# Kernel tuning notes

Hardware: AMD Instinct MI355X
Metric: run time of the kernel (lower is better)

The kernel has to match this reference:

```python
import jax, jax.numpy as jnp
import numpy as np

N, E, G = 50000, 640000, 256
NODE_IN, EDGE_IN, EXT_IN = 32, 16, 8
H, L = 128, 3
BN_EPS = 1e-5


def _linear_init(key, fan_in, fan_out):
    kw, kb = jax.random.split(key)
    s = 1.0 / np.sqrt(fan_in)
    w = jax.random.uniform(kw, (fan_in, fan_out), minval=-s, maxval=s, dtype=jnp.float32)
    b = jax.random.uniform(kb, (fan_out,), minval=-s, maxval=s, dtype=jnp.float32)
    return w, b


def setup_inputs() -> dict:
    key = jax.random.key(0)
    ks = jax.random.split(key, 16)
    x = jax.random.normal(ks[0], (N, NODE_IN), dtype=jnp.float32)
    edge_index = jax.random.randint(ks[1], (2, E), 0, N)
    edge_attr = jax.random.normal(ks[2], (E, EDGE_IN), dtype=jnp.float32)
    batch = jnp.sort(jax.random.randint(ks[3], (N,), 0, G))
    externals = jax.random.normal(ks[4], (G, EXT_IN), dtype=jnp.float32)

    node_w, node_b = _linear_init(ks[5], NODE_IN, H)
    ee_w1, ee_b1 = _linear_init(ks[6], EDGE_IN, H)
    ee_w2, ee_b2 = _linear_init(ks[7], H, H)
    # stacked per-layer GINEConv MLP params: [L, H, H] / [L, H]
    cks = jax.random.split(ks[8], 2 * L)
    cw1, cb1, cw2, cb2 = [], [], [], []
    for l in range(L):
        w1, b1 = _linear_init(cks[2 * l], H, H)
        w2, b2 = _linear_init(cks[2 * l + 1], H, H)
        cw1.append(w1); cb1.append(b1); cw2.append(w2); cb2.append(b2)
    conv_w1 = jnp.stack(cw1); conv_b1 = jnp.stack(cb1)
    conv_w2 = jnp.stack(cw2); conv_b2 = jnp.stack(cb2)
    bn_gamma = jnp.ones((L, H), dtype=jnp.float32)
    bn_beta = jnp.zeros((L, H), dtype=jnp.float32)
    ext_w1, ext_b1 = _linear_init(ks[9], EXT_IN, H)
    ext_w2, ext_b2 = _linear_init(ks[10], H, H)
    reg_w1, reg_b1 = _linear_init(ks[11], 2 * H, H)
    reg_w2, reg_b2 = _linear_init(ks[12], H, 1)

    return dict(x=x, edge_attr=edge_attr, externals=externals,
                node_w=node_w, node_b=node_b,
                ee_w1=ee_w1, ee_b1=ee_b1, ee_w2=ee_w2, ee_b2=ee_b2,
                conv_w1=conv_w1, conv_b1=conv_b1, conv_w2=conv_w2, conv_b2=conv_b2,
                bn_gamma=bn_gamma, bn_beta=bn_beta,
                ext_w1=ext_w1, ext_b1=ext_b1, ext_w2=ext_w2, ext_b2=ext_b2,
                reg_w1=reg_w1, reg_b1=reg_b1, reg_w2=reg_w2, reg_b2=reg_b2,
                edge_index=edge_index, batch=batch, num_graphs=G)


def reference(x, edge_attr, externals,
              node_w, node_b, ee_w1, ee_b1, ee_w2, ee_b2,
              conv_w1, conv_b1, conv_w2, conv_b2, bn_gamma, bn_beta,
              ext_w1, ext_b1, ext_w2, ext_b2,
              reg_w1, reg_b1, reg_w2, reg_b2,
              edge_index, batch, num_graphs):
    n = x.shape[0]
    src, dst = edge_index[0], edge_index[1]
    h = x @ node_w + node_b                                      # [N,H]
    e = jax.nn.relu(edge_attr @ ee_w1 + ee_b1) @ ee_w2 + ee_b2   # [E,H]
    for l in range(conv_w1.shape[0]):
        # GINEConv (eps=0): aggr = sum_j relu(x_j + e_ij); out = MLP(x_i + aggr)
        msg = jax.nn.relu(h[src] + e)                            # gather + add + relu [E,H]
        aggr = jax.ops.segment_sum(msg, dst, num_segments=n)     # scatter-add [N,H]
        z = h + aggr
        z = jax.nn.relu(z @ conv_w1[l] + conv_b1[l]) @ conv_w2[l] + conv_b2[l]
        # BatchNorm1d (batch statistics)
        mean = z.mean(axis=0)
        var = z.var(axis=0)
        z = (z - mean) * jax.lax.rsqrt(var + BN_EPS) * bn_gamma[l] + bn_beta[l]
        h = jax.nn.relu(z)                                       # dropout = identity (eval)
    # global mean pool over graphs
    gsum = jax.ops.segment_sum(h, batch, num_segments=num_graphs)
    cnt = jax.ops.segment_sum(jnp.ones((n, 1), h.dtype), batch, num_segments=num_graphs)
    graph_emb = gsum / jnp.maximum(cnt, 1.0)
    ext = jax.nn.relu(externals @ ext_w1 + ext_b1) @ ext_w2 + ext_b2
    comb = jnp.concatenate([graph_emb, ext], axis=-1)            # [G,2H]
    out = jax.nn.relu(comb @ reg_w1 + reg_b1) @ reg_w2 + reg_b2  # [G,1]
    return out.squeeze(-1)
```

## Files before the change

### kernel.cpp

```cpp
#include <hip/hip_runtime.h>

typedef __bf16 bf16_t;
typedef __bf16 bf16x8 __attribute__((ext_vector_type(8)));
typedef __bf16 bf16x4 __attribute__((ext_vector_type(4)));
typedef __bf16 bf16x2 __attribute__((ext_vector_type(2)));
typedef float  f32x4  __attribute__((ext_vector_type(4)));

#define MFMA16(a, b, c) __builtin_amdgcn_mfma_f32_16x16x32_bf16((a), (b), (c), 0, 0, 0)

__global__ __launch_bounds__(256) void prep_all_kernel(
    const float* __restrict__ nw,  const float* __restrict__ ew1,
    const float* __restrict__ ew2, const float* __restrict__ cw1,
    const float* __restrict__ cw2,
    bf16_t* __restrict__ nwt,  bf16_t* __restrict__ ew1t,
    bf16_t* __restrict__ ew2t, bf16_t* __restrict__ cw1t,
    bf16_t* __restrict__ cw2t)
{
    int b = blockIdx.x;
    const float* W; bf16_t* O; int Kact, KP, lb;
    if (b < 16)       { W = nw;  O = nwt;  Kact = 32;  KP = 32;  lb = b; }
    else if (b < 32)  { W = ew1; O = ew1t; Kact = 16;  KP = 32;  lb = b - 16; }
    else if (b < 96)  { W = ew2; O = ew2t; Kact = 128; KP = 128; lb = b - 32; }
    else if (b < 288) { int l = (b - 96) / 64;  W = cw1 + l * 16384; O = cw1t + l * 16384;
                        Kact = 128; KP = 128; lb = (b - 96) % 64; }
    else              { int l = (b - 288) / 64; W = cw2 + l * 16384; O = cw2t + l * 16384;
                        Kact = 128; KP = 128; lb = (b - 288) % 64; }
    int idx = lb * 256 + threadIdx.x;
    if (idx >= 128 * KP) return;
    int j    = idx & 7;
    int lane = (idx >> 3) & 63;
    int ct   = (idx >> 9) & 7;
    int kc   = idx >> 12;
    int n = ct * 16 + (lane & 15);
    int k = kc * 32 + (lane >> 4) * 8 + j;
    O[idx] = (bf16_t)((k < Kact) ? W[k * 128 + n] : 0.0f);
}

__global__ __launch_bounds__(256) void hist_kernel(const int* __restrict__ ei,
                                                   int* __restrict__ deg, int E,
                                                   const float* __restrict__ ea) {
    int t = blockIdx.x * 256 + threadIdx.x;
    if (t < E) {
        atomicAdd(&deg[ei[(long)E + t]], 1);
        float w0 = ea[(long)t * 16];
        float w1 = ea[(long)t * 16 + 8];
        asm volatile("" :: "v"(w0), "v"(w1));
    }
}

__global__ __launch_bounds__(256) void scanA_kernel(const int* __restrict__ deg,
                                                    int* __restrict__ partials,
                                                    int* __restrict__ bsums, int N) {
    __shared__ int s[256];
    int b = blockIdx.x, t = threadIdx.x;
    int base = b * 1024 + t * 4;
    int v0 = (base + 0 < N) ? deg[base + 0] : 0;
    int v1 = (base + 1 < N) ? deg[base + 1] : 0;
    int v2 = (base + 2 < N) ? deg[base + 2] : 0;
    int v3 = (base + 3 < N) ? deg[base + 3] : 0;
    int local = v0 + v1 + v2 + v3;
    s[t] = local;
    __syncthreads();
    for (int off = 1; off < 256; off <<= 1) {
        int v = (t >= off) ? s[t - off] : 0;
        __syncthreads();
        s[t] += v;
        __syncthreads();
    }
    int excl = s[t] - local;
    if (base + 0 < N) partials[base + 0] = excl;
    if (base + 1 < N) partials[base + 1] = excl + v0;
    if (base + 2 < N) partials[base + 2] = excl + v0 + v1;
    if (base + 3 < N) partials[base + 3] = excl + v0 + v1 + v2;
    if (t == 255) bsums[b] = s[255];
}

__global__ __launch_bounds__(256) void scanB_kernel(const int* __restrict__ bsums,
                                                    int* __restrict__ boff,
                                                    int* __restrict__ rowptr,
                                                    int NB, int N) {
    __shared__ int s[256];
    int t = threadIdx.x;
    int local = (t < NB) ? bsums[t] : 0;
    s[t] = local;
    __syncthreads();
    for (int off = 1; off < 256; off <<= 1) {
        int v = (t >= off) ? s[t - off] : 0;
        __syncthreads();
        s[t] += v;
        __syncthreads();
    }
    if (t < NB) boff[t] = s[t] - local;
    if (t == NB - 1) rowptr[N] = s[t];
}

__global__ __launch_bounds__(256) void scanC_kernel(const int* __restrict__ partials,
                                                    const int* __restrict__ boff,
                                                    int* __restrict__ rowptr,
                                                    int* __restrict__ cursor, int N) {
    int i = blockIdx.x * 256 + threadIdx.x;
    if (i >= N) return;
    int v = partials[i] + boff[i >> 10];
    rowptr[i] = v;
    cursor[i] = v;
}

__global__ __launch_bounds__(256) void scatter_kernel(const int* __restrict__ ei,
                                                      int* __restrict__ cursor,
                                                      int* __restrict__ srcp,
                                                      int* __restrict__ eorig, int E) {
    int t = blockIdx.x * 256 + threadIdx.x;
    if (t >= E) return;
    int d = ei[(long)E + t];
    int pos = atomicAdd(&cursor[d], 1);
    srcp[pos] = ei[t];
    eorig[pos] = t;
}

__global__ __launch_bounds__(256) void node_enc_kernel(
    const float* __restrict__ A, int M,
    const bf16_t* __restrict__ Ws, const float* __restrict__ bias,
    bf16_t* __restrict__ outp)
{
    constexpr int S = 136;
    __shared__ bf16_t T[128 * S];

    const int  tid  = threadIdx.x;
    const int  wv   = tid >> 6, lane = tid & 63;
    const long row0 = (long)blockIdx.x * 128;
    const int  l16  = lane & 15, quad = lane >> 4;

    {
        int r  = wv * 32 + (lane >> 1);
        long gr = row0 + r;
        int c0 = (lane & 1) * 16;
#pragma unroll
        for (int q = 0; q < 4; ++q) {
            float4 v = make_float4(0.f, 0.f, 0.f, 0.f);
            if (gr < M) v = *(const float4*)(A + gr * 32 + c0 + q * 4);
            bf16_t* d = &T[r * S + c0 + q * 4];
            d[0] = (bf16_t)v.x; d[1] = (bf16_t)v.y; d[2] = (bf16_t)v.z; d[3] = (bf16_t)v.w;
        }
    }

    f32x4 acc[2][8];
#pragma unroll
    for (int r = 0; r < 2; r++)
#pragma unroll
        for (int c = 0; c < 8; c++) acc[r][c] = (f32x4){0.f, 0.f, 0.f, 0.f};

    {
        bf16x8 af0 = *(const bf16x8*)&T[(wv * 32 + l16) * S + quad * 8];
        bf16x8 af1 = *(const bf16x8*)&T[(wv * 32 + 16 + l16) * S + quad * 8];
#pragma unroll
        for (int c = 0; c < 8; c++) {
            bf16x8 bfr = *(const bf16x8*)&Ws[((c * 64) + lane) * 8];
            acc[0][c] = MFMA16(af0, bfr, acc[0][c]);
            acc[1][c] = MFMA16(af1, bfr, acc[1][c]);
        }
    }

#pragma unroll
    for (int r = 0; r < 2; r++) {
        int mrow = wv * 32 + r * 16 + quad * 4;
#pragma unroll
        for (int c = 0; c < 8; c++) {
            int col = c * 16 + l16;
            float bb = bias[col];
#pragma unroll
            for (int q = 0; q < 4; q++)
                T[(mrow + q) * S + col] = (bf16_t)(acc[r][c][q] + bb);
        }
    }

#pragma unroll
    for (int it = 0; it < 8; ++it) {
        int idx = it * 64 + lane;
        int row = wv * 32 + (idx >> 4);
        int seg = idx & 15;
        long grow = row0 + row;
        if (grow < M)
            *(uint4*)&outp[grow * 128 + seg * 8] = *(const uint4*)&T[row * S + seg * 8];
    }
}

__global__ __launch_bounds__(256) void edge_mlp_kernel(
    const float* __restrict__ A, int M,
    const bf16_t* __restrict__ Ws1, const float* __restrict__ b1,
    const bf16_t* __restrict__ Ws2, const float* __restrict__ b2,
    const int* __restrict__ eorig, bf16_t* __restrict__ outp)
{
    constexpr int S = 136;
    __shared__ bf16_t T[64 * S];

    const int  tid  = threadIdx.x;
    const int  wv   = tid >> 6, lane = tid & 63;
    const long row0 = (long)blockIdx.x * 64;
    const int  l16  = lane & 15, quad = lane >> 4;

    {
        int  r  = wv * 16 + (lane >> 2);
        long gr = row0 + r;
        float4 v = make_float4(0.f, 0.f, 0.f, 0.f);
        if (gr < M) {
            long eo = eorig[gr];
            v = *(const float4*)(A + eo * 16 + (lane & 3) * 4);
        }
        bf16_t* d = &T[r * S + (lane & 3) * 4];
        d[0] = (bf16_t)v.x; d[1] = (bf16_t)v.y; d[2] = (bf16_t)v.z; d[3] = (bf16_t)v.w;
    }

    f32x4 acc[8];
#pragma unroll
    for (int c = 0; c < 8; c++) acc[c] = (f32x4){0.f, 0.f, 0.f, 0.f};

    {
        bf16x8 af;
#pragma unroll
        for (int j = 0; j < 8; ++j) af[j] = (bf16_t)0.f;
        if (quad < 2) af = *(const bf16x8*)&T[(wv * 16 + l16) * S + quad * 8];
#pragma unroll
        for (int c = 0; c < 8; c++) {
            bf16x8 bfr = *(const bf16x8*)&Ws1[((c * 64) + lane) * 8];
            acc[c] = MFMA16(af, bfr, acc[c]);
        }
    }

    const int mbase = wv * 16 + quad * 4;

#pragma unroll
    for (int c = 0; c < 8; c++) {
        int col = c * 16 + l16;
        float bb = b1[col];
#pragma unroll
        for (int q = 0; q < 4; q++)
            T[(mbase + q) * S + col] = (bf16_t)fmaxf(acc[c][q] + bb, 0.f);
    }

#pragma unroll
    for (int c = 0; c < 8; c++) acc[c] = (f32x4){0.f, 0.f, 0.f, 0.f};

#pragma unroll
    for (int kc = 0; kc < 4; ++kc) {
        bf16x8 af = *(const bf16x8*)&T[(wv * 16 + l16) * S + kc * 32 + quad * 8];
#pragma unroll
        for (int c = 0; c < 8; c++) {
            bf16x8 bfr = *(const bf16x8*)&Ws2[(((kc * 8 + c) * 64) + lane) * 8];
            acc[c] = MFMA16(af, bfr, acc[c]);
        }
    }

#pragma unroll
    for (int c = 0; c < 8; c++) {
        int col = c * 16 + l16;
        float bb = b2[col];
#pragma unroll
        for (int q = 0; q < 4; q++)
            T[(mbase + q) * S + col] = (bf16_t)(acc[c][q] + bb);
    }

#pragma unroll
    for (int it = 0; it < 4; ++it) {
        int idx = it * 64 + lane;
        int row = wv * 16 + (idx >> 4);
        int seg = idx & 15;
        long grow = row0 + row;
        if (grow < M)
            *(uint4*)&outp[grow * 128 + seg * 8] = *(const uint4*)&T[row * S + seg * 8];
    }
}

template <int BN>
__global__ __launch_bounds__(512) void aggr_conv_kernel(
    const bf16_t* __restrict__ xin,
    const float* __restrict__ bns_prev,
    const float* __restrict__ gamma, const float* __restrict__ beta,
    const bf16_t* __restrict__ e,
    const int* __restrict__ rowptr, const int* __restrict__ srcp, int M,
    const bf16_t* __restrict__ Ws1, const float* __restrict__ b1,
    const bf16_t* __restrict__ Ws2, const float* __restrict__ b2,
    bf16_t* __restrict__ zout, float* __restrict__ bn_out)
{
    constexpr int S = 136;
    __shared__ bf16_t T[64 * S];

    const int  tid  = threadIdx.x;
    const int  wv   = tid >> 6, lane = tid & 63;
    const int  tw   = wv >> 1, sub = wv & 1;
    const long row0 = (long)blockIdx.x * 64;

    float sc0 = 1.f, sh0 = 0.f, sc1 = 1.f, sh1 = 0.f;
    if (BN) {
        const float invM = 1.f / (float)M;
        int c = lane * 2;
        float m0 = bns_prev[c] * invM;
        float v0 = bns_prev[128 + c] * invM - m0 * m0;
        float i0 = rsqrtf(v0 + 1e-5f);
        sc0 = gamma[c] * i0; sh0 = beta[c] - m0 * sc0;
        float m1 = bns_prev[c + 1] * invM;
        float v1 = bns_prev[128 + c + 1] * invM - m1 * m1;
        float i1 = rsqrtf(v1 + 1e-5f);
        sc1 = gamma[c + 1] * i1; sh1 = beta[c + 1] - m1 * sc1;
    }

    const long nbase = row0 + tw * 16 + sub * 8;
    int rpv = 0;
    {
        long idx = nbase + lane;
        if (idx > M) idx = M;
        if (lane <= 8) rpv = rowptr[idx];
    }

    int sv;
    {
        int b0 = __shfl(rpv, 0), e0 = __shfl(rpv, 1);
        sv = (b0 + lane < e0) ? srcp[b0 + lane] : 0;
    }

#pragma unroll 1
    for (int r8 = 0; r8 < 8; ++r8) {
        const int  r   = tw * 16 + sub * 8 + r8;
        const long n   = row0 + r;
        const int  beg = __shfl(rpv, r8);
        const int  end = __shfl(rpv, r8 + 1);
        int svc = sv;
        if (r8 < 7) {
            int nb = __shfl(rpv, r8 + 1), ne = __shfl(rpv, r8 + 2);
            sv = (nb + lane < ne) ? srcp[nb + lane] : 0;
        }
        float ax = 0.f, ay = 0.f;
        if (n < M) {
            bf16x2 xv = *(const bf16x2*)(xin + n * 128 + lane * 2);
            ax = BN ? fmaxf((float)xv[0] * sc0 + sh0, 0.f) : (float)xv[0];
            ay = BN ? fmaxf((float)xv[1] * sc1 + sh1, 0.f) : (float)xv[1];
            for (int base = beg; base < end; base += 64) {
                int cnt = min(64, end - base);
                int svv = (base == beg) ? svc
                                        : ((base + lane < end) ? srcp[base + lane] : 0);
                int j = 0;
                for (; j + 3 < cnt; j += 4) {
                    int s0 = __shfl(svv, j),     s1 = __shfl(svv, j + 1);
                    int s2 = __shfl(svv, j + 2), s3 = __shfl(svv, j + 3);
                    bf16x2 x0 = *(const bf16x2*)(xin + (long)s0 * 128 + lane * 2);
                    bf16x2 x1 = *(const bf16x2*)(xin + (long)s1 * 128 + lane * 2);
                    bf16x2 x2 = *(const bf16x2*)(xin + (long)s2 * 128 + lane * 2);
                    bf16x2 x3 = *(const bf16x2*)(xin + (long)s3 * 128 + lane * 2);
                    bf16x2 e0 = *(const bf16x2*)(e + (long)(base + j + 0) * 128 + lane * 2);
                    bf16x2 e1 = *(const bf16x2*)(e + (long)(base + j + 1) * 128 + lane * 2);
                    bf16x2 e2 = *(const bf16x2*)(e + (long)(base + j + 2) * 128 + lane * 2);
                    bf16x2 e3 = *(const bf16x2*)(e + (long)(base + j + 3) * 128 + lane * 2);
                    float hx, hy;
                    hx = BN ? fmaxf((float)x0[0] * sc0 + sh0, 0.f) : (float)x0[0];
                    hy = BN ? fmaxf((float)x0[1] * sc1 + sh1, 0.f) : (float)x0[1];
                    ax += fmaxf(hx + (float)e0[0], 0.f);
                    ay += fmaxf(hy + (float)e0[1], 0.f);
                    hx = BN ? fmaxf((float)x1[0] * sc0 + sh0, 0.f) : (float)x1[0];
                    hy = BN ? fmaxf((float)x1[1] * sc1 + sh1, 0.f) : (float)x1[1];
                    ax += fmaxf(hx + (float)e1[0], 0.f);
                    ay += fmaxf(hy + (float)e1[1], 0.f);
                    hx = BN ? fmaxf((float)x2[0] * sc0 + sh0, 0.f) : (float)x2[0];
                    hy = BN ? fmaxf((float)x2[1] * sc1 + sh1, 0.f) : (float)x2[1];
                    ax += fmaxf(hx + (float)e2[0], 0.f);
                    ay += fmaxf(hy + (float)e2[1], 0.f);
                    hx = BN ? fmaxf((float)x3[0] * sc0 + sh0, 0.f) : (float)x3[0];
                    hy = BN ? fmaxf((float)x3[1] * sc1 + sh1, 0.f) : (float)x3[1];
                    ax += fmaxf(hx + (float)e3[0], 0.f);
                    ay += fmaxf(hy + (float)e3[1], 0.f);
                }
                for (; j < cnt; ++j) {
                    int s0 = __shfl(svv, j);
                    bf16x2 x0 = *(const bf16x2*)(xin + (long)s0 * 128 + lane * 2);
                    bf16x2 e0 = *(const bf16x2*)(e + (long)(base + j) * 128 + lane * 2);
                    float hx = BN ? fmaxf((float)x0[0] * sc0 + sh0, 0.f) : (float)x0[0];
                    float hy = BN ? fmaxf((float)x0[1] * sc1 + sh1, 0.f) : (float)x0[1];
                    ax += fmaxf(hx + (float)e0[0], 0.f);
                    ay += fmaxf(hy + (float)e0[1], 0.f);
                }
            }
        }
        bf16x2 o; o[0] = (bf16_t)ax; o[1] = (bf16_t)ay;
        *(bf16x2*)&T[r * S + lane * 2] = o;
    }
    __syncthreads();

    if (sub == 0) {
        const int l16 = lane & 15, quad = lane >> 4;
        const int mbase = tw * 16 + quad * 4;

        f32x4 acc[8];
#pragma unroll
        for (int c = 0; c < 8; c++) acc[c] = (f32x4){0.f, 0.f, 0.f, 0.f};

#pragma unroll
        for (int kc = 0; kc < 4; ++kc) {
            bf16x8 af = *(const bf16x8*)&T[(tw * 16 + l16) * S + kc * 32 + quad * 8];
#pragma unroll
            for (int c = 0; c < 8; c++) {
                bf16x8 bfr = *(const bf16x8*)&Ws1[(((kc * 8 + c) * 64) + lane) * 8];
                acc[c] = MFMA16(af, bfr, acc[c]);
            }
        }

#pragma unroll
        for (int c = 0; c < 8; c++) {
            int col = c * 16 + l16;
            float bb = b1[col];
#pragma unroll
            for (int q = 0; q < 4; q++)
                T[(mbase + q) * S + col] = (bf16_t)fmaxf(acc[c][q] + bb, 0.f);
        }

#pragma unroll
        for (int c = 0; c < 8; c++) acc[c] = (f32x4){0.f, 0.f, 0.f, 0.f};

#pragma unroll
        for (int kc = 0; kc < 4; ++kc) {
            bf16x8 af = *(const bf16x8*)&T[(tw * 16 + l16) * S + kc * 32 + quad * 8];
#pragma unroll
            for (int c = 0; c < 8; c++) {
                bf16x8 bfr = *(const bf16x8*)&Ws2[(((kc * 8 + c) * 64) + lane) * 8];
                acc[c] = MFMA16(af, bfr, acc[c]);
            }
        }

        float ssum[8], ssq[8];
#pragma unroll
        for (int c = 0; c < 8; c++) {
            int col = c * 16 + l16;
            float bb = b2[col];
            float s = 0.f, s2 = 0.f;
#pragma unroll
            for (int q = 0; q < 4; q++) {
                float v = acc[c][q] + bb;
                T[(mbase + q) * S + col] = (bf16_t)v;
                if (row0 + mbase + q < M) { s += v; s2 += v * v; }
            }
            s  += __shfl_xor(s, 16);  s  += __shfl_xor(s, 32);
            s2 += __shfl_xor(s2, 16); s2 += __shfl_xor(s2, 32);
            ssum[c] = s; ssq[c] = s2;
        }

#pragma unroll
        for (int it = 0; it < 4; ++it) {
            int idx = it * 64 + lane;
            int row = tw * 16 + (idx >> 4);
            int seg = idx & 15;
            long grow = row0 + row;
            if (grow < M)
                *(uint4*)&zout[grow * 128 + seg * 8] = *(const uint4*)&T[row * S + seg * 8];
        }

        float* wred = (float*)&T[(size_t)(tw * 16) * S];
        if (quad == 0) {
#pragma unroll
            for (int c = 0; c < 8; c++) {
                int col = c * 16 + l16;
                wred[col]       = ssum[c];
                wred[128 + col] = ssq[c];
            }
        }
    }
    __syncthreads();
    if (tid < 128) {
        float s = 0.f, s2 = 0.f;
#pragma unroll
        for (int w = 0; w < 4; ++w) {
            const float* wr = (const float*)&T[(size_t)(w * 16) * S];
            s  += wr[tid];
            s2 += wr[128 + tid];
        }
        atomicAdd(&bn_out[tid], s);
        atomicAdd(&bn_out[128 + tid], s2);
    }
}

__global__ __launch_bounds__(128) void pool_kernel(
    const bf16_t* __restrict__ z, const float* __restrict__ bns,
    const float* __restrict__ gamma, const float* __restrict__ beta,
    const int* __restrict__ batch,
    float* __restrict__ gsum, float* __restrict__ cnt, int N)
{
    int c = threadIdx.x;
    float mean = bns[c] / (float)N;
    float var  = bns[128 + c] / (float)N - mean * mean;
    float inv  = rsqrtf(var + 1e-5f);
    float sc   = gamma[c] * inv;
    float sh   = beta[c] - mean * sc;
    int n0 = blockIdx.x * 32;
    int n1 = min(n0 + 32, N);
    float acc = 0.f;
    int cur = -1, rc = 0;
    for (int n = n0; n < n1; ++n) {
        int g = batch[n];
        if (g != cur) {
            if (cur >= 0) {
                atomicAdd(&gsum[(long)cur * 128 + c], acc);
                if (c == 0) atomicAdd(&cnt[cur], (float)rc);
            }
            cur = g; acc = 0.f; rc = 0;
        }
        acc += fmaxf((float)z[(long)n * 128 + c] * sc + sh, 0.f);
        rc++;
    }
    if (cur >= 0) {
        atomicAdd(&gsum[(long)cur * 128 + c], acc);
        if (c == 0) atomicAdd(&cnt[cur], (float)rc);
    }
}

__global__ __launch_bounds__(128) void head_kernel(
    const float* __restrict__ gsum, const float* __restrict__ cnt,
    const float* __restrict__ ext_in,
    const float* __restrict__ ew1, const float* __restrict__ eb1,
    const float* __restrict__ ew2, const float* __restrict__ eb2,
    const float* __restrict__ rw1, const float* __restrict__ rb1,
    const float* __restrict__ rw2, const float* __restrict__ rb2,
    float* __restrict__ out)
{
    int g = blockIdx.x, c = threadIdx.x;
    __shared__ float sx[8];
    __shared__ float h1[128];
    __shared__ float comb[256];
    __shared__ float red[128];

    if (c < 8) sx[c] = ext_in[g * 8 + c];
    __syncthreads();
    float a = eb1[c];
#pragma unroll
    for (int k = 0; k < 8; k++) a += sx[k] * ew1[k * 128 + c];
    h1[c] = fmaxf(a, 0.f);
    __syncthreads();
    float b = eb2[c];
    for (int k = 0; k < 128; k++) b += h1[k] * ew2[k * 128 + c];
    comb[c]       = gsum[(long)g * 128 + c] / fmaxf(cnt[g], 1.0f);
    comb[128 + c] = b;
    __syncthreads();
    float r = rb1[c];
    for (int k = 0; k < 256; k++) r += comb[k] * rw1[k * 128 + c];
    r = fmaxf(r, 0.f);
    red[c] = r * rw2[c];
    __syncthreads();
    if (c == 0) {
        float s = rb2[0];
        for (int k = 0; k < 128; k++) s += red[k];
        out[g] = s;
    }
}

extern "C" void kernel_launch(void* const* d_in, const int* in_sizes, int n_in,
                              void* d_out, int out_size, void* d_ws, size_t ws_size,
                              hipStream_t stream)
{
    const float* x         = (const float*)d_in[0];
    const float* edge_attr = (const float*)d_in[1];
    const float* externals = (const float*)d_in[2];
    const float* node_w    = (const float*)d_in[3];
    const float* node_b    = (const float*)d_in[4];
    const float* ee_w1     = (const float*)d_in[5];
    const float* ee_b1     = (const float*)d_in[6];
    const float* ee_w2     = (const float*)d_in[7];
    const float* ee_b2     = (const float*)d_in[8];
    const float* conv_w1   = (const float*)d_in[9];
    const float* conv_b1   = (const float*)d_in[10];
    const float* conv_w2   = (const float*)d_in[11];
    const float* conv_b2   = (const float*)d_in[12];
    const float* bn_gamma  = (const float*)d_in[13];
    const float* bn_beta   = (const float*)d_in[14];
    const float* ext_w1    = (const float*)d_in[15];
    const float* ext_b1    = (const float*)d_in[16];
    const float* ext_w2    = (const float*)d_in[17];
    const float* ext_b2    = (const float*)d_in[18];
    const float* reg_w1    = (const float*)d_in[19];
    const float* reg_b1    = (const float*)d_in[20];
    const float* reg_w2    = (const float*)d_in[21];
    const float* reg_b2    = (const float*)d_in[22];
    const int* edge_index  = (const int*)d_in[23];
    const int* batch       = (const int*)d_in[24];

    const int N = in_sizes[0] / 32;
    const int E = in_sizes[1] / 16;
    const int G = in_sizes[2] / 8;
    const int NB = (N + 1023) / 1024;

    char* p = (char*)d_ws;
    auto alloc = [&](size_t bytes) -> void* {
        void* r = (void*)p;
        p += (bytes + 255) & ~(size_t)255;
        return r;
    };
    bf16_t* h       = (bf16_t*)alloc((size_t)N * 128 * 2);
    bf16_t* zA      = (bf16_t*)alloc((size_t)N * 128 * 2);
    bf16_t* zB      = (bf16_t*)alloc((size_t)N * 128 * 2);
    bf16_t* ebuf    = (bf16_t*)alloc((size_t)E * 128 * 2);
    int*    deg     = (int*)alloc((size_t)N * 4);
    int*    rowptr  = (int*)alloc(((size_t)N + 1) * 4);
    int*    cursor  = (int*)alloc((size_t)N * 4);
    int*    partials= (int*)alloc((size_t)N * 4);
    int*    bsums   = (int*)alloc((size_t)NB * 4);
    int*    boff    = (int*)alloc((size_t)NB * 4);
    int*    srcp    = (int*)alloc((size_t)E * 4);
    int*    eorig   = (int*)alloc((size_t)E * 4);
    bf16_t* node_wt = (bf16_t*)alloc(128 * 32 * 2);
    bf16_t* ee_w1t  = (bf16_t*)alloc(128 * 32 * 2);
    bf16_t* ee_w2t  = (bf16_t*)alloc(128 * 128 * 2);
    bf16_t* cw1t    = (bf16_t*)alloc(3 * 128 * 128 * 2);
    bf16_t* cw2t    = (bf16_t*)alloc(3 * 128 * 128 * 2);
    float*  bns     = (float*)alloc(3 * 256 * 4);
    float*  gsum    = (float*)alloc((size_t)G * 128 * 4);
    float*  cnt     = (float*)alloc((size_t)G * 4);

    hipMemsetAsync(deg, 0, (size_t)N * 4, stream);
    hipMemsetAsync(bns, 0, 3 * 256 * 4, stream);
    hist_kernel<<<(E + 255) / 256, 256, 0, stream>>>(edge_index, deg, E, edge_attr);
    scanA_kernel<<<NB, 256, 0, stream>>>(deg, partials, bsums, N);
    scanB_kernel<<<1, 256, 0, stream>>>(bsums, boff, rowptr, NB, N);
    scanC_kernel<<<(N + 255) / 256, 256, 0, stream>>>(partials, boff, rowptr, cursor, N);
    scatter_kernel<<<(E + 255) / 256, 256, 0, stream>>>(edge_index, cursor, srcp, eorig, E);

    prep_all_kernel<<<480, 256, 0, stream>>>(node_w, ee_w1, ee_w2, conv_w1, conv_w2,
                                             node_wt, ee_w1t, ee_w2t, cw1t, cw2t);

    node_enc_kernel<<<(N + 127) / 128, 256, 0, stream>>>(x, N, node_wt, node_b, h);

    edge_mlp_kernel<<<(E + 63) / 64, 256, 0, stream>>>(
        edge_attr, E, ee_w1t, ee_b1, ee_w2t, ee_b2, eorig, ebuf);

    const int nblk = (N + 63) / 64;
    aggr_conv_kernel<0><<<nblk, 512, 0, stream>>>(
        h, nullptr, nullptr, nullptr, ebuf, rowptr, srcp, N,
        cw1t + 0 * 16384, conv_b1 + 0 * 128, cw2t + 0 * 16384, conv_b2 + 0 * 128,
        zA, bns + 0);
    aggr_conv_kernel<1><<<nblk, 512, 0, stream>>>(
        zA, bns + 0, bn_gamma + 0, bn_beta + 0, ebuf, rowptr, srcp, N,
        cw1t + 1 * 16384, conv_b1 + 1 * 128, cw2t + 1 * 16384, conv_b2 + 1 * 128,
        zB, bns + 256);
    aggr_conv_kernel<1><<<nblk, 512, 0, stream>>>(
        zB, bns + 256, bn_gamma + 128, bn_beta + 128, ebuf, rowptr, srcp, N,
        cw1t + 2 * 16384, conv_b1 + 2 * 128, cw2t + 2 * 16384, conv_b2 + 2 * 128,
        zA, bns + 512);

    hipMemsetAsync(gsum, 0, (size_t)G * 128 * 4, stream);
    hipMemsetAsync(cnt, 0, (size_t)G * 4, stream);
    pool_kernel<<<(N + 31) / 32, 128, 0, stream>>>(zA, bns + 512, bn_gamma + 256, bn_beta + 256,
                                                   batch, gsum, cnt, N);
    head_kernel<<<G, 128, 0, stream>>>(gsum, cnt, externals,
                                       ext_w1, ext_b1, ext_w2, ext_b2,
                                       reg_w1, reg_b1, reg_w2, reg_b2,
                                       (float*)d_out);
}
```

Baseline: 578.6 us.

## Materialize BN+ReLU activations and gather 16-byte rows with four edges per wave

Moves the BatchNorm-apply-and-ReLU of the previous layer out of the per-edge gather into a separate elementwise kernel that writes a normalized bf16 buffer. The aggregation loop now has each quarter-wave handle a different edge, with 16-byte vector loads per lane instead of 4-byte ones, followed by a cross-quad shuffle reduction. The goal is fewer, wider memory transactions on the gather and less per-edge ALU work. The cost is two extra kernel launches and an extra full pass over the node features, and the srcp prefetch across rows is dropped.

```diff
diff --git a/kernel.cpp b/kernel.cpp
--- a/kernel.cpp
+++ b/kernel.cpp
@@ -270,11 +270,33 @@
     }
 }
 
-template <int BN>
+__global__ __launch_bounds__(256) void bnx_kernel(
+    const bf16_t* __restrict__ z, const float* __restrict__ bns,
+    const float* __restrict__ gamma, const float* __restrict__ beta,
+    bf16_t* __restrict__ hbuf, int N)
+{
+    long t = (long)blockIdx.x * 256 + threadIdx.x;
+    long i0 = t * 8;
+    if (i0 >= (long)N * 128) return;
+    int c = (int)(i0 & 127);
+    const float invN = 1.f / (float)N;
+    bf16x8 v = *(const bf16x8*)(z + i0);
+    bf16x8 o;
+#pragma unroll
+    for (int u = 0; u < 8; ++u) {
+        int cc = c + u;
+        float m  = bns[cc] * invN;
+        float va = bns[128 + cc] * invN - m * m;
+        float iv = rsqrtf(va + 1e-5f);
+        float sc = gamma[cc] * iv;
+        float sh = beta[cc] - m * sc;
+        o[u] = (bf16_t)fmaxf((float)v[u] * sc + sh, 0.f);
+    }
+    *(bf16x8*)(hbuf + i0) = o;
+}
+
 __global__ __launch_bounds__(512) void aggr_conv_kernel(
     const bf16_t* __restrict__ xin,
-    const float* __restrict__ bns_prev,
-    const float* __restrict__ gamma, const float* __restrict__ beta,
     const bf16_t* __restrict__ e,
     const int* __restrict__ rowptr, const int* __restrict__ srcp, int M,
     const bf16_t* __restrict__ Ws1, const float* __restrict__ b1,
@@ -287,21 +309,8 @@
     const int  tid  = threadIdx.x;
     const int  wv   = tid >> 6, lane = tid & 63;
     const int  tw   = wv >> 1, sub = wv & 1;
+    const int  l16  = lane & 15, quad = lane >> 4;
     const long row0 = (long)blockIdx.x * 64;
-
-    float sc0 = 1.f, sh0 = 0.f, sc1 = 1.f, sh1 = 0.f;
-    if (BN) {
-        const float invM = 1.f / (float)M;
-        int c = lane * 2;
-        float m0 = bns_prev[c] * invM;
-        float v0 = bns_prev[128 + c] * invM - m0 * m0;
-        float i0 = rsqrtf(v0 + 1e-5f);
-        sc0 = gamma[c] * i0; sh0 = beta[c] - m0 * sc0;
-        float m1 = bns_prev[c + 1] * invM;
-        float v1 = bns_prev[128 + c + 1] * invM - m1 * m1;
-        float i1 = rsqrtf(v1 + 1e-5f);
-        sc1 = gamma[c + 1] * i1; sh1 = beta[c + 1] - m1 * sc1;
-    }
 
     const long nbase = row0 + tw * 16 + sub * 8;
     int rpv = 0;
@@ -311,80 +320,53 @@
         if (lane <= 8) rpv = rowptr[idx];
     }
 
-    int sv;
-    {
-        int b0 = __shfl(rpv, 0), e0 = __shfl(rpv, 1);
-        sv = (b0 + lane < e0) ? srcp[b0 + lane] : 0;
-    }
-
 #pragma unroll 1
     for (int r8 = 0; r8 < 8; ++r8) {
         const int  r   = tw * 16 + sub * 8 + r8;
         const long n   = row0 + r;
         const int  beg = __shfl(rpv, r8);
         const int  end = __shfl(rpv, r8 + 1);
-        int svc = sv;
-        if (r8 < 7) {
-            int nb = __shfl(rpv, r8 + 1), ne = __shfl(rpv, r8 + 2);
-            sv = (nb + lane < ne) ? srcp[nb + lane] : 0;
-        }
-        float ax = 0.f, ay = 0.f;
+        float a[8];
+#pragma unroll
+        for (int u = 0; u < 8; ++u) a[u] = 0.f;
         if (n < M) {
-            bf16x2 xv = *(const bf16x2*)(xin + n * 128 + lane * 2);
-            ax = BN ? fmaxf((float)xv[0] * sc0 + sh0, 0.f) : (float)xv[0];
-            ay = BN ? fmaxf((float)xv[1] * sc1 + sh1, 0.f) : (float)xv[1];
             for (int base = beg; base < end; base += 64) {
                 int cnt = min(64, end - base);
-                int svv = (base == beg) ? svc
-                                        : ((base + lane < end) ? srcp[base + lane] : 0);
-                int j = 0;
-                for (; j + 3 < cnt; j += 4) {
-                    int s0 = __shfl(svv, j),     s1 = __shfl(svv, j + 1);
-                    int s2 = __shfl(svv, j + 2), s3 = __shfl(svv, j + 3);
-                    bf16x2 x0 = *(const bf16x2*)(xin + (long)s0 * 128 + lane * 2);
-                    bf16x2 x1 = *(const bf16x2*)(xin + (long)s1 * 128 + lane * 2);
-                    bf16x2 x2 = *(const bf16x2*)(xin + (long)s2 * 128 + lane * 2);
-                    bf16x2 x3 = *(const bf16x2*)(xin + (long)s3 * 128 + lane * 2);
-                    bf16x2 e0 = *(const bf16x2*)(e + (long)(base + j + 0) * 128 + lane * 2);
-                    bf16x2 e1 = *(const bf16x2*)(e + (long)(base + j + 1) * 128 + lane * 2);
-                    bf16x2 e2 = *(const bf16x2*)(e + (long)(base + j + 2) * 128 + lane * 2);
-                    bf16x2 e3 = *(const bf16x2*)(e + (long)(base + j + 3) * 128 + lane * 2);
-                    float hx, hy;
-                    hx = BN ? fmaxf((float)x0[0] * sc0 + sh0, 0.f) : (float)x0[0];
-                    hy = BN ? fmaxf((float)x0[1] * sc1 + sh1, 0.f) : (float)x0[1];
-                    ax += fmaxf(hx + (float)e0[0], 0.f);
-                    ay += fmaxf(hy + (float)e0[1], 0.f);
-                    hx = BN ? fmaxf((float)x1[0] * sc0 + sh0, 0.f) : (float)x1[0];
-                    hy = BN ? fmaxf((float)x1[1] * sc1 + sh1, 0.f) : (float)x1[1];
-                    ax += fmaxf(hx + (float)e1[0], 0.f);
-                    ay += fmaxf(hy + (float)e1[1], 0.f);
-                    hx = BN ? fmaxf((float)x2[0] * sc0 + sh0, 0.f) : (float)x2[0];
-                    hy = BN ? fmaxf((float)x2[1] * sc1 + sh1, 0.f) : (float)x2[1];
-                    ax += fmaxf(hx + (float)e2[0], 0.f);
-                    ay += fmaxf(hy + (float)e2[1], 0.f);
-                    hx = BN ? fmaxf((float)x3[0] * sc0 + sh0, 0.f) : (float)x3[0];
-                    hy = BN ? fmaxf((float)x3[1] * sc1 + sh1, 0.f) : (float)x3[1];
-                    ax += fmaxf(hx + (float)e3[0], 0.f);
-                    ay += fmaxf(hy + (float)e3[1], 0.f);
-                }
-                for (; j < cnt; ++j) {
-                    int s0 = __shfl(svv, j);
-                    bf16x2 x0 = *(const bf16x2*)(xin + (long)s0 * 128 + lane * 2);
-                    bf16x2 e0 = *(const bf16x2*)(e + (long)(base + j) * 128 + lane * 2);
-                    float hx = BN ? fmaxf((float)x0[0] * sc0 + sh0, 0.f) : (float)x0[0];
-                    float hy = BN ? fmaxf((float)x0[1] * sc1 + sh1, 0.f) : (float)x0[1];
-                    ax += fmaxf(hx + (float)e0[0], 0.f);
-                    ay += fmaxf(hy + (float)e0[1], 0.f);
+                int sv  = (base + lane < end) ? srcp[base + lane] : 0;
+                int ng  = (cnt + 3) >> 2;
+                for (int jj = 0; jj < ng; ++jj) {
+                    int  ei = jj * 4 + quad;
+                    bool vv = ei < cnt;
+                    int  ec = vv ? ei : (cnt - 1);
+                    int  src = __shfl(sv, ec);
+                    bf16x8 xv = *(const bf16x8*)(xin + (long)src * 128 + l16 * 8);
+                    bf16x8 ev = *(const bf16x8*)(e + (long)(base + ec) * 128 + l16 * 8);
+#pragma unroll
+                    for (int u = 0; u < 8; ++u) {
+                        float t = fmaxf((float)xv[u] + (float)ev[u], 0.f);
+                        a[u] += vv ? t : 0.f;
+                    }
                 }
             }
-        }
-        bf16x2 o; o[0] = (bf16_t)ax; o[1] = (bf16_t)ay;
-        *(bf16x2*)&T[r * S + lane * 2] = o;
+#pragma unroll
+            for (int u = 0; u < 8; ++u) {
+                a[u] += __shfl_xor(a[u], 16);
+                a[u] += __shfl_xor(a[u], 32);
+            }
+            bf16x8 xs = *(const bf16x8*)(xin + n * 128 + l16 * 8);
+#pragma unroll
+            for (int u = 0; u < 8; ++u) a[u] += (float)xs[u];
+        }
+        if (quad == 0) {
+            bf16x8 o;
+#pragma unroll
+            for (int u = 0; u < 8; ++u) o[u] = (bf16_t)a[u];
+            *(uint4*)&T[r * S + l16 * 8] = *(uint4*)&o;
+        }
     }
     __syncthreads();
 
     if (sub == 0) {
-        const int l16 = lane & 15, quad = lane >> 4;
         const int mbase = tw * 16 + quad * 4;
 
         f32x4 acc[8];
@@ -591,6 +573,7 @@
     bf16_t* h       = (bf16_t*)alloc((size_t)N * 128 * 2);
     bf16_t* zA      = (bf16_t*)alloc((size_t)N * 128 * 2);
     bf16_t* zB      = (bf16_t*)alloc((size_t)N * 128 * 2);
+    bf16_t* hb      = (bf16_t*)alloc((size_t)N * 128 * 2);
     bf16_t* ebuf    = (bf16_t*)alloc((size_t)E * 128 * 2);
     int*    deg     = (int*)alloc((size_t)N * 4);
     int*    rowptr  = (int*)alloc(((size_t)N + 1) * 4);
@@ -626,16 +609,19 @@
         edge_attr, E, ee_w1t, ee_b1, ee_w2t, ee_b2, eorig, ebuf);
 
     const int nblk = (N + 63) / 64;
-    aggr_conv_kernel<0><<<nblk, 512, 0, stream>>>(
-        h, nullptr, nullptr, nullptr, ebuf, rowptr, srcp, N,
+    const int bblk = ((N * 128 / 8) + 255) / 256;
+    aggr_conv_kernel<<<nblk, 512, 0, stream>>>(
+        h, ebuf, rowptr, srcp, N,
         cw1t + 0 * 16384, conv_b1 + 0 * 128, cw2t + 0 * 16384, conv_b2 + 0 * 128,
         zA, bns + 0);
-    aggr_conv_kernel<1><<<nblk, 512, 0, stream>>>(
-        zA, bns + 0, bn_gamma + 0, bn_beta + 0, ebuf, rowptr, srcp, N,
+    bnx_kernel<<<bblk, 256, 0, stream>>>(zA, bns + 0, bn_gamma + 0, bn_beta + 0, hb, N);
+    aggr_conv_kernel<<<nblk, 512, 0, stream>>>(
+        hb, ebuf, rowptr, srcp, N,
         cw1t + 1 * 16384, conv_b1 + 1 * 128, cw2t + 1 * 16384, conv_b2 + 1 * 128,
         zB, bns + 256);
-    aggr_conv_kernel<1><<<nblk, 512, 0, stream>>>(
-        zB, bns + 256, bn_gamma + 128, bn_beta + 128, ebuf, rowptr, srcp, N,
+    bnx_kernel<<<bblk, 256, 0, stream>>>(zB, bns + 256, bn_gamma + 128, bn_beta + 128, hb, N);
+    aggr_conv_kernel<<<nblk, 512, 0, stream>>>(
+        hb, ebuf, rowptr, srcp, N,
         cw1t + 2 * 16384, conv_b1 + 2 * 128, cw2t + 2 * 16384, conv_b2 + 2 * 128,
         zA, bns + 512);
 
```

Result: slower. 612.8 us (+5.9%).
